# Kernel tuning notes

Hardware: AMD Instinct MI355X
Metric: run time of the kernel (lower is better)

Reference implementation:

```python
import jax, jax.numpy as jnp
import numpy as np

CHUNK = 64
NORM_EPS = 1e-5
DENOM_EPS = 1.0
B, S, HID, H = 4, 4096, 1024, 8
D = HID // H  # 128


def rmsnorm(x, w, eps=NORM_EPS):
    var = jnp.mean(x * x, axis=-1, keepdims=True)
    return x * jax.lax.rsqrt(var + eps) * w


def chunked_linear_attn(q, k, v):
    # q,k,v: [B,S,H,D]; causal linear attention o_s = q_s @ sum_{t<=s} k_t^T v_t
    b, s, h, d = q.shape
    n = s // CHUNK
    def to_chunks(x):
        return x.reshape(b, n, CHUNK, h, d).transpose(1, 0, 3, 2, 4)  # [N,B,H,C,D]
    qc, kc, vc = to_chunks(q), to_chunks(k), to_chunks(v)
    mask = jnp.tril(jnp.ones((CHUNK, CHUNK), dtype=q.dtype))
    def step(state, inp):
        qq, kk, vv = inp  # [B,H,C,D]
        inter = jnp.einsum('bhcd,bhde->bhce', qq, state)
        scores = jnp.einsum('bhcd,bhed->bhce', qq, kk) * mask  # causal intra-chunk
        intra = jnp.einsum('bhce,bhed->bhcd', scores, vv)
        state = state + jnp.einsum('bhcd,bhce->bhde', kk, vv)
        return state, inter + intra
    init = jnp.zeros((b, h, d, d), dtype=q.dtype)
    _, o = jax.lax.scan(step, init, (qc, kc, vc))  # [N,B,H,C,D]
    return o.transpose(1, 0, 3, 2, 4).reshape(b, s, h, d)


def setup_inputs() -> dict:
    key = jax.random.key(0)
    k0, k1, k2, k3, k4 = jax.random.split(key, 5)
    hidden_states = jax.random.normal(k0, (B, S, HID), dtype=jnp.float32)
    Wq = jax.random.normal(k1, (HID, HID), dtype=jnp.float32) * 0.02
    Wk = jax.random.normal(k2, (HID, HID), dtype=jnp.float32) * 0.02
    Wv = jax.random.normal(k3, (HID, HID), dtype=jnp.float32) * 0.02
    Wo = jax.random.normal(k4, (HID, HID), dtype=jnp.float32) * 0.02
    norm_w = jnp.ones((D,), dtype=jnp.float32)
    return {"hidden_states": hidden_states, "Wq": Wq, "Wk": Wk, "Wv": Wv, "Wo": Wo, "norm_w": norm_w}


def reference(hidden_states, Wq, Wk, Wv, Wo, norm_w):
    b, s, _ = hidden_states.shape
    q = jnp.einsum('bsd,ed->bse', hidden_states, Wq).reshape(b, s, H, D)
    k = jnp.einsum('bsd,ed->bse', hidden_states, Wk).reshape(b, s, H, D)
    v = jnp.einsum('bsd,ed->bse', hidden_states, Wv).reshape(b, s, H, D)
    # feature_map='identity', norm_q/norm_k=False
    o = chunked_linear_attn(q, k, v)  # [B,S,H,D]
    z = jnp.cumsum(k, axis=1)
    denom = jnp.maximum(jnp.abs(jnp.sum(q * z, axis=-1)), DENOM_EPS)[..., None]
    o = o / denom
    o = rmsnorm(o, norm_w)
    o = o.reshape(b, s, H * D)
    return jnp.einsum('bse,de->bsd', o, Wo)
```

## Files before the change

### kernel.cpp

```cpp
#include <hip/hip_runtime.h>
#include <stdint.h>

typedef __bf16 bf16x8 __attribute__((ext_vector_type(8)));
typedef float  f32x4  __attribute__((ext_vector_type(4)));

static __device__ __forceinline__ void gload16(const void* g, void* l) {
  __builtin_amdgcn_global_load_lds((__attribute__((address_space(1))) void*)g,
                                   (__attribute__((address_space(3))) void*)l,
                                   16, 0, 0);
}

static __device__ __forceinline__ f32x4 mfma16(bf16x8 a, bf16x8 b, f32x4 c) {
  return __builtin_amdgcn_mfma_f32_16x16x32_bf16(a, b, c, 0, 0, 0);
}

__global__ __launch_bounds__(256) void cast8_k(const float* __restrict__ in,
                                               __bf16* __restrict__ out) {
  const size_t i = ((size_t)blockIdx.x * 256 + threadIdx.x) * 8;
  const float4 v0 = *(const float4*)(in + i);
  const float4 v1 = *(const float4*)(in + i + 4);
  bf16x8 o;
  o[0] = (__bf16)v0.x; o[1] = (__bf16)v0.y; o[2] = (__bf16)v0.z; o[3] = (__bf16)v0.w;
  o[4] = (__bf16)v1.x; o[5] = (__bf16)v1.y; o[6] = (__bf16)v1.z; o[7] = (__bf16)v1.w;
  *(bf16x8*)(out + i) = o;
}

__global__ __launch_bounds__(256) void castw_k(const float* __restrict__ w0, const float* __restrict__ w1,
                                               const float* __restrict__ w2, const float* __restrict__ w3,
                                               __bf16* __restrict__ o0, __bf16* __restrict__ o1,
                                               __bf16* __restrict__ o2, __bf16* __restrict__ o3) {
  const float* in; __bf16* out;
  switch (blockIdx.y) {
    case 0: in = w0; out = o0; break;
    case 1: in = w1; out = o1; break;
    case 2: in = w2; out = o2; break;
    default: in = w3; out = o3; break;
  }
  const size_t i = ((size_t)blockIdx.x * 256 + threadIdx.x) * 8;
  const float4 v0 = *(const float4*)(in + i);
  const float4 v1 = *(const float4*)(in + i + 4);
  bf16x8 o;
  o[0] = (__bf16)v0.x; o[1] = (__bf16)v0.y; o[2] = (__bf16)v0.z; o[3] = (__bf16)v0.w;
  o[4] = (__bf16)v1.x; o[5] = (__bf16)v1.y; o[6] = (__bf16)v1.z; o[7] = (__bf16)v1.w;
  *(bf16x8*)(out + i) = o;
}

__global__ __launch_bounds__(256)
void gemm_qkv_k(const __bf16* __restrict__ A,
                const __bf16* __restrict__ Bq, const __bf16* __restrict__ Bk, const __bf16* __restrict__ Bv,
                __bf16* __restrict__ Qo, __bf16* __restrict__ Ko,
                __bf16* __restrict__ Kt, __bf16* __restrict__ Vt) {
  alignas(16) __shared__ __bf16 sh[128 * 136];
  __bf16* As = sh;
  __bf16* Bs = sh + 128 * 32;
  __bf16* Ts = sh;

  const int tid = threadIdx.x;
  const int flat = blockIdx.x + (blockIdx.y << 3) + (blockIdx.z << 10);
  const int sf = (flat & 7) * 384 + (flat >> 3);
  const int z = sf >> 10;
  const int rem = sf & 1023;
  const int m0 = (rem >> 3) * 128;
  const int n0 = (rem & 7) * 128;

  const __bf16* W = (z == 0) ? Bq : (z == 1) ? Bk : Bv;
  const int l = tid & 63, w = tid >> 6;
  const int wr = (w >> 1) * 64, wc = (w & 1) * 64;
  const int lr = l & 15, lk = (l >> 4) * 8;
  const int srow = tid >> 2, scol = (tid & 3) * 8;

  f32x4 acc[4][4] = {};
  for (int k0 = 0; k0 < 1024; k0 += 32) {
    gload16(A + (size_t)(m0 + srow) * 1024 + k0 + scol, &As[srow * 32 + scol]);
    gload16(A + (size_t)(m0 + 64 + srow) * 1024 + k0 + scol, &As[(64 + srow) * 32 + scol]);
    gload16(W + (size_t)(n0 + srow) * 1024 + k0 + scol, &Bs[srow * 32 + scol]);
    gload16(W + (size_t)(n0 + 64 + srow) * 1024 + k0 + scol, &Bs[(64 + srow) * 32 + scol]);
    __syncthreads();
    bf16x8 af[4], bfr[4];
#pragma unroll
    for (int mt = 0; mt < 4; ++mt) af[mt] = *(const bf16x8*)&As[(wr + mt * 16 + lr) * 32 + lk];
#pragma unroll
    for (int nt = 0; nt < 4; ++nt) bfr[nt] = *(const bf16x8*)&Bs[(wc + nt * 16 + lr) * 32 + lk];
#pragma unroll
    for (int mt = 0; mt < 4; ++mt)
#pragma unroll
      for (int nt = 0; nt < 4; ++nt)
        acc[mt][nt] = mfma16(af[mt], bfr[nt], acc[mt][nt]);
    __syncthreads();
  }

  if (z <= 1) {
    __bf16* R = (z == 0) ? Qo : Ko;
#pragma unroll
    for (int mt = 0; mt < 4; ++mt)
#pragma unroll
      for (int r = 0; r < 4; ++r) {
        const int m = m0 + wr + mt * 16 + (l >> 4) * 4 + r;
#pragma unroll
        for (int nt = 0; nt < 4; ++nt)
          R[(size_t)m * 1024 + n0 + wc + nt * 16 + lr] = (__bf16)acc[mt][nt][r];
      }
  }
  if (z >= 1) {
#pragma unroll
    for (int mt = 0; mt < 4; ++mt)
#pragma unroll
      for (int r = 0; r < 4; ++r) {
        const int m = wr + mt * 16 + (l >> 4) * 4 + r;
#pragma unroll
        for (int nt = 0; nt < 4; ++nt) {
          const int n = wc + nt * 16 + lr;
          Ts[n * 136 + m] = (__bf16)acc[mt][nt][r];
        }
      }
    __syncthreads();
    const int bb = m0 >> 12, s0 = m0 & 4095, hh = n0 >> 7;
    __bf16* T = (z == 1) ? Kt : Vt;
    const size_t tbase = ((size_t)((bb * 8 + hh) * 128)) * 4096 + s0;
#pragma unroll
    for (int it = 0; it < 8; ++it) {
      const int dd = it * 16 + (tid >> 4), s8 = (tid & 15) * 8;
      *(bf16x8*)(T + tbase + (size_t)dd * 4096 + s8) = *(const bf16x8*)&Ts[dd * 136 + s8];
    }
  }
}

__global__ __launch_bounds__(256)
void gemm_out_k(const __bf16* __restrict__ A, const __bf16* __restrict__ W,
                float* __restrict__ Co) {
  alignas(16) __shared__ __bf16 As[128 * 32];
  alignas(16) __shared__ __bf16 Bs[128 * 32];
  const int tid = threadIdx.x;
  const int flat = blockIdx.x + (blockIdx.y << 3);
  const int sf = (flat & 7) * 128 + (flat >> 3);
  const int m0 = (sf >> 3) * 128;
  const int n0 = (sf & 7) * 128;
  const int l = tid & 63, w = tid >> 6;
  const int wr = (w >> 1) * 64, wc = (w & 1) * 64;
  const int lr = l & 15, lk = (l >> 4) * 8;
  const int srow = tid >> 2, scol = (tid & 3) * 8;

  f32x4 acc[4][4] = {};
  for (int k0 = 0; k0 < 1024; k0 += 32) {
    gload16(A + (size_t)(m0 + srow) * 1024 + k0 + scol, &As[srow * 32 + scol]);
    gload16(A + (size_t)(m0 + 64 + srow) * 1024 + k0 + scol, &As[(64 + srow) * 32 + scol]);
    gload16(W + (size_t)(n0 + srow) * 1024 + k0 + scol, &Bs[srow * 32 + scol]);
    gload16(W + (size_t)(n0 + 64 + srow) * 1024 + k0 + scol, &Bs[(64 + srow) * 32 + scol]);
    __syncthreads();
    bf16x8 af[4], bfr[4];
#pragma unroll
    for (int mt = 0; mt < 4; ++mt) af[mt] = *(const bf16x8*)&As[(wr + mt * 16 + lr) * 32 + lk];
#pragma unroll
    for (int nt = 0; nt < 4; ++nt) bfr[nt] = *(const bf16x8*)&Bs[(wc + nt * 16 + lr) * 32 + lk];
#pragma unroll
    for (int mt = 0; mt < 4; ++mt)
#pragma unroll
      for (int nt = 0; nt < 4; ++nt)
        acc[mt][nt] = mfma16(af[mt], bfr[nt], acc[mt][nt]);
    __syncthreads();
  }
#pragma unroll
  for (int mt = 0; mt < 4; ++mt)
#pragma unroll
    for (int r = 0; r < 4; ++r) {
      const int m = m0 + wr + mt * 16 + (l >> 4) * 4 + r;
#pragma unroll
      for (int nt = 0; nt < 4; ++nt) {
        const int n = n0 + wc + nt * 16 + lr;
        Co[(size_t)m * 1024 + n] = acc[mt][nt][r];
      }
    }
}

__global__ __launch_bounds__(128)
void z1_k(const __bf16* __restrict__ K, float* __restrict__ zc) {
  const int c = blockIdx.x, bh = blockIdx.y;
  const int bb = bh >> 3, hh = bh & 7;
  const int d = threadIdx.x;
  float a = 0.0f;
  for (int t = 0; t < 64; ++t)
    a += (float)K[((size_t)(bb * 4096 + c * 64 + t)) * 1024 + hh * 128 + d];
  zc[(size_t)(bh * 64 + c) * 128 + d] = a;
}

__global__ __launch_bounds__(128)
void z2_k(float* __restrict__ zc) {
  const int bh = blockIdx.x;
  const int d = threadIdx.x;
  float run = 0.0f;
  for (int cc = 0; cc < 64; ++cc) {
    float* p = zc + (size_t)(bh * 64 + cc) * 128 + d;
    const float old = *p;
    *p = run;
    run += old;
  }
}

__global__ __launch_bounds__(256)
void passA_k(const __bf16* __restrict__ Kt, const __bf16* __restrict__ Vt,
             __bf16* __restrict__ Sc) {
  const int c = blockIdx.x, bh = blockIdx.y;
  const int tid = threadIdx.x, l = tid & 63, w = tid >> 6;
  const int wr = (w >> 1) * 64, wc = (w & 1) * 64;
  const int lr = l & 15, lk = (l >> 4) * 8;
  f32x4 acc[4][4] = {};
#pragma unroll
  for (int kk = 0; kk < 2; ++kk) {
    const int t = c * 64 + kk * 32 + lk;
    bf16x8 av[4], bk[4];
#pragma unroll
    for (int mt = 0; mt < 4; ++mt)
      av[mt] = *(const bf16x8*)(Vt + ((size_t)(bh * 128 + wr + mt * 16 + lr)) * 4096 + t);
#pragma unroll
    for (int nt = 0; nt < 4; ++nt)
      bk[nt] = *(const bf16x8*)(Kt + ((size_t)(bh * 128 + wc + nt * 16 + lr)) * 4096 + t);
#pragma unroll
    for (int mt = 0; mt < 4; ++mt)
#pragma unroll
      for (int nt = 0; nt < 4; ++nt)
        acc[mt][nt] = mfma16(av[mt], bk[nt], acc[mt][nt]);
  }
  const size_t sbase = ((size_t)(bh * 64 + c)) << 14;
#pragma unroll
  for (int mt = 0; mt < 4; ++mt)
#pragma unroll
    for (int r = 0; r < 4; ++r) {
      const int e = wr + mt * 16 + (l >> 4) * 4 + r;
#pragma unroll
      for (int nt = 0; nt < 4; ++nt) {
        const int d = wc + nt * 16 + lr;
        Sc[sbase + (size_t)e * 128 + d] = (__bf16)acc[mt][nt][r];
      }
    }
}

__global__ __launch_bounds__(256)
void passB_k(__bf16* __restrict__ Sc) {
  const int bh = blockIdx.y;
  const int idx = blockIdx.x * 256 + threadIdx.x;
  float run = 0.0f;
  for (int cc = 0; cc < 64; ++cc) {
    __bf16* p = Sc + (((size_t)(bh * 64 + cc)) << 14) + idx;
    const float old = (float)*p;
    *p = (__bf16)run;
    run += old;
  }
}

__global__ __launch_bounds__(256)
void passC_k(const __bf16* __restrict__ Q, const __bf16* __restrict__ K,
             const __bf16* __restrict__ Vt, const __bf16* __restrict__ Sp,
             const float* __restrict__ zp, const float* __restrict__ nw,
             __bf16* __restrict__ O) {
  alignas(16) __shared__ __bf16 ScL[64 * 72];
  alignas(16) __shared__ float OL[64 * 132];
  alignas(16) __shared__ float zPL[128];
  alignas(16) __shared__ float nwL[128];
  alignas(16) __shared__ float dnL[64];
  const int c = blockIdx.x, bh = blockIdx.y;
  const int bb = bh >> 3, hh = bh & 7;
  const int tid = threadIdx.x, l = tid & 63, wv = tid >> 6;
  const int lr = l & 15, lk = (l >> 4) * 8;
  if (tid < 128) zPL[tid] = zp[(size_t)(bh * 64 + c) * 128 + tid];
  else nwL[tid - 128] = nw[tid - 128];

  const size_t qbase = ((size_t)(bb * 4096 + c * 64)) * 1024 + hh * 128;
  const size_t sbase = ((size_t)(bh * 64 + c)) << 14;

  f32x4 accO[4][2] = {};
  f32x4 accS[4] = {};
#pragma unroll
  for (int kk = 0; kk < 4; ++kk) {
    const int dof = kk * 32 + lk;
    bf16x8 aQ[4], bS[2], bK;
#pragma unroll
    for (int mt = 0; mt < 4; ++mt)
      aQ[mt] = *(const bf16x8*)(Q + qbase + (size_t)(mt * 16 + lr) * 1024 + dof);
#pragma unroll
    for (int nt = 0; nt < 2; ++nt)
      bS[nt] = *(const bf16x8*)(Sp + sbase + (size_t)(wv * 32 + nt * 16 + lr) * 128 + dof);
    bK = *(const bf16x8*)(K + qbase + (size_t)(wv * 16 + lr) * 1024 + dof);
#pragma unroll
    for (int mt = 0; mt < 4; ++mt) {
      accS[mt] = mfma16(aQ[mt], bK, accS[mt]);
#pragma unroll
      for (int nt = 0; nt < 2; ++nt)
        accO[mt][nt] = mfma16(aQ[mt], bS[nt], accO[mt][nt]);
    }
  }
#pragma unroll
  for (int mt = 0; mt < 4; ++mt)
#pragma unroll
    for (int r = 0; r < 4; ++r) {
      const int srow = mt * 16 + (l >> 4) * 4 + r;
      const int tcol = wv * 16 + lr;
      ScL[srow * 72 + tcol] = (__bf16)((tcol <= srow) ? accS[mt][r] : 0.0f);
    }
  __syncthreads();
#pragma unroll
  for (int kk2 = 0; kk2 < 2; ++kk2) {
    const int tof = kk2 * 32 + lk;
    bf16x8 aS[4], bV[2];
#pragma unroll
    for (int mt = 0; mt < 4; ++mt) aS[mt] = *(const bf16x8*)&ScL[(mt * 16 + lr) * 72 + tof];
#pragma unroll
    for (int nt = 0; nt < 2; ++nt)
      bV[nt] = *(const bf16x8*)(Vt + ((size_t)(bh * 128 + wv * 32 + nt * 16 + lr)) * 4096 + c * 64 + tof);
#pragma unroll
    for (int mt = 0; mt < 4; ++mt)
#pragma unroll
      for (int nt = 0; nt < 2; ++nt)
        accO[mt][nt] = mfma16(aS[mt], bV[nt], accO[mt][nt]);
  }
  if (tid < 64) {
    float rs = 0.0f;
    for (int t = 0; t < 64; ++t) rs += (float)ScL[tid * 72 + t];
    float qz = 0.0f;
    const __bf16* qrow = Q + qbase + (size_t)tid * 1024;
#pragma unroll
    for (int j = 0; j < 16; ++j) {
      const bf16x8 q8 = *(const bf16x8*)(qrow + j * 8);
#pragma unroll
      for (int i = 0; i < 8; ++i) qz += (float)q8[i] * zPL[j * 8 + i];
    }
    dnL[tid] = fmaxf(fabsf(qz + rs), 1.0f);
  }
  __syncthreads();
#pragma unroll
  for (int mt = 0; mt < 4; ++mt)
#pragma unroll
    for (int r = 0; r < 4; ++r) {
      const int row = mt * 16 + (l >> 4) * 4 + r;
#pragma unroll
      for (int nt = 0; nt < 2; ++nt) {
        const int col = wv * 32 + nt * 16 + lr;
        OL[row * 132 + col] = accO[mt][nt][r] / dnL[row];
      }
    }
  __syncthreads();
  const int s = tid >> 2, e0 = (tid & 3) * 32;
  float ss = 0.0f;
  for (int i = 0; i < 32; ++i) { const float v = OL[s * 132 + e0 + i]; ss += v * v; }
  ss += __shfl_xor(ss, 1);
  ss += __shfl_xor(ss, 2);
  const float scale = rsqrtf(ss * (1.0f / 128.0f) + 1e-5f);
  __bf16* orow = O + qbase + (size_t)s * 1024 + e0;
#pragma unroll
  for (int i8 = 0; i8 < 4; ++i8) {
    bf16x8 ov;
#pragma unroll
    for (int j = 0; j < 8; ++j) {
      const int e = e0 + i8 * 8 + j;
      ov[j] = (__bf16)(OL[s * 132 + e] * scale * nwL[e]);
    }
    *(bf16x8*)(orow + i8 * 8) = ov;
  }
}

extern "C" void kernel_launch(void* const* d_in, const int* in_sizes, int n_in,
                              void* d_out, int out_size, void* d_ws, size_t ws_size,
                              hipStream_t stream) {
  (void)in_sizes; (void)n_in; (void)out_size; (void)ws_size;
  const float* hid = (const float*)d_in[0];
  const float* Wq  = (const float*)d_in[1];
  const float* Wk  = (const float*)d_in[2];
  const float* Wv  = (const float*)d_in[3];
  const float* Wo  = (const float*)d_in[4];
  const float* nw  = (const float*)d_in[5];

  char* ws = (char*)d_ws;
  size_t off = 0;
  auto nxt = [&](size_t bytes) -> char* {
    char* p = ws + off;
    off += (bytes + 255) & ~(size_t)255;
    return p;
  };
  __bf16* hA  = (__bf16*)nxt(33554432);
  __bf16* wqB = (__bf16*)nxt(2097152);
  __bf16* wkB = (__bf16*)nxt(2097152);
  __bf16* wvB = (__bf16*)nxt(2097152);
  __bf16* woB = (__bf16*)nxt(2097152);
  __bf16* Qb  = (__bf16*)nxt(33554432);
  __bf16* Kb  = (__bf16*)nxt(33554432);
  __bf16* Ktb = (__bf16*)nxt(33554432);
  __bf16* Vtb = (__bf16*)nxt(33554432);
  __bf16* Scb = (__bf16*)nxt(67108864);
  float*  zcb = (float*)nxt(1048576);
  __bf16* Ob  = hA;

  cast8_k<<<8192, 256, 0, stream>>>(hid, hA);
  castw_k<<<dim3(512, 4), 256, 0, stream>>>(Wq, Wk, Wv, Wo, wqB, wkB, wvB, woB);
  gemm_qkv_k<<<dim3(8, 128, 3), 256, 0, stream>>>(hA, wqB, wkB, wvB, Qb, Kb, Ktb, Vtb);
  z1_k<<<dim3(64, 32), 128, 0, stream>>>(Kb, zcb);
  passA_k<<<dim3(64, 32), 256, 0, stream>>>(Ktb, Vtb, Scb);
  passB_k<<<dim3(64, 32), 256, 0, stream>>>(Scb);
  z2_k<<<32, 128, 0, stream>>>(zcb);
  passC_k<<<dim3(64, 32), 256, 0, stream>>>(Qb, Kb, Vtb, Scb, zcb, nw, Ob);
  gemm_out_k<<<dim3(8, 128), 256, 0, stream>>>(Ob, woB, (float*)d_out);
}
```

Baseline: 418.7 us.

## Replace QKV and output GEMMs with 256x256 double-buffered pipelined MFMA kernels

The QKV and output projection GEMMs move from 128x128 tiles with a single LDS buffer and K-step 32 to 256x256 tiles with 512 threads and K-step 64. The new kernels use double-buffered, XOR-swizzled LDS loaded via global_load_lds, with the MFMA work split into four phases interleaved with prefetch, explicit waitcnt/barriers and setprio. The epilogue now stages results through LDS for coalesced 16-byte stores. The goal is more data reuse per tile and overlap of global loads with MFMA. In exchange it needs 128KB of dynamic LDS and heavy register use, and hand-tuned synchronization that is risky to get wrong.

```diff
diff --git a/kernel.cpp b/kernel.cpp
--- a/kernel.cpp
+++ b/kernel.cpp
@@ -13,6 +13,8 @@
 static __device__ __forceinline__ f32x4 mfma16(bf16x8 a, bf16x8 b, f32x4 c) {
   return __builtin_amdgcn_mfma_f32_16x16x32_bf16(a, b, c, 0, 0, 0);
 }
+
+#define MEMFENCE asm volatile("" ::: "memory")
 
 __global__ __launch_bounds__(256) void cast8_k(const float* __restrict__ in,
                                                __bf16* __restrict__ out) {
@@ -45,131 +47,240 @@
   *(bf16x8*)(out + i) = o;
 }
 
-__global__ __launch_bounds__(256)
-void gemm_qkv_k(const __bf16* __restrict__ A,
-                const __bf16* __restrict__ Bq, const __bf16* __restrict__ Bk, const __bf16* __restrict__ Bv,
-                __bf16* __restrict__ Qo, __bf16* __restrict__ Ko,
-                __bf16* __restrict__ Kt, __bf16* __restrict__ Vt) {
-  alignas(16) __shared__ __bf16 sh[128 * 136];
-  __bf16* As = sh;
-  __bf16* Bs = sh + 128 * 32;
-  __bf16* Ts = sh;
-
+static __device__ __forceinline__ void kloop256(
+    const __bf16* __restrict__ A, const __bf16* __restrict__ W,
+    int m0, int n0, __bf16* sh, int tid, f32x4 acc[8][4]) {
+  const int l = tid & 63;
+  const int wv = tid >> 6;
+  const int wm = wv >> 2, wn = wv & 3;
+  const int lo = l & 15, kq = l >> 4;
+
+  auto SA = [&](int kt, int h) {
+#pragma unroll
+    for (int j = 0; j < 2; ++j) {
+      const int p = j * 512 + tid;
+      const int r = p >> 3, sl = p & 7;
+      const int grow = m0 + h * 64 + (r & 63) + (r >> 6) * 128;
+      gload16(A + (size_t)grow * 1024 + (kt << 6) + ((sl ^ (r & 7)) << 3),
+              sh + (kt & 1) * 32768 + h * 8192 + p * 8);
+    }
+  };
+  auto SB = [&](int kt, int h) {
+#pragma unroll
+    for (int j = 0; j < 2; ++j) {
+      const int p = j * 512 + tid;
+      const int r = p >> 3, sl = p & 7;
+      const int grow = n0 + h * 32 + (r & 31) + (r >> 5) * 64;
+      gload16(W + (size_t)grow * 1024 + (kt << 6) + ((sl ^ (r & 7)) << 3),
+              sh + (kt & 1) * 32768 + 16384 + h * 8192 + p * 8);
+    }
+  };
+  auto LDA = [&](int cur, int mh, int mi, int ks) -> bf16x8 {
+    const int r = wm * 64 + mi * 16 + lo;
+    return *(const bf16x8*)&sh[cur * 32768 + mh * 8192 + r * 64 + (((ks * 4 + kq) ^ (r & 7)) << 3)];
+  };
+  auto LDB = [&](int cur, int nh, int ni, int ks) -> bf16x8 {
+    const int r = wn * 32 + ni * 16 + lo;
+    return *(const bf16x8*)&sh[cur * 32768 + 16384 + nh * 8192 + r * 64 + (((ks * 4 + kq) ^ (r & 7)) << 3)];
+  };
+
+  SA(0, 0); SB(0, 0); SB(0, 1); SA(0, 1);
+  SA(1, 0); SB(1, 1); SA(1, 1);
+  MEMFENCE;
+  asm volatile("s_waitcnt vmcnt(6)" ::: "memory");
+  __builtin_amdgcn_s_barrier();
+
+  bf16x8 a[4][2], b[2][2], b2[2][2];
+#pragma unroll 2
+  for (int t = 0; t < 16; ++t) {
+    const int cur = t & 1;
+#pragma unroll
+    for (int mi = 0; mi < 4; ++mi)
+#pragma unroll
+      for (int ks = 0; ks < 2; ++ks) a[mi][ks] = LDA(cur, 0, mi, ks);
+#pragma unroll
+    for (int ni = 0; ni < 2; ++ni)
+#pragma unroll
+      for (int ks = 0; ks < 2; ++ks) b[ni][ks] = LDB(cur, 0, ni, ks);
+    if (t + 1 < 16) SB(t + 1, 0);
+    MEMFENCE;
+    __builtin_amdgcn_s_barrier();
+    asm volatile("s_waitcnt lgkmcnt(0)" ::: "memory");
+    __builtin_amdgcn_sched_barrier(0);
+    __builtin_amdgcn_s_setprio(1);
+#pragma unroll
+    for (int mi = 0; mi < 4; ++mi)
+#pragma unroll
+      for (int ni = 0; ni < 2; ++ni)
+#pragma unroll
+        for (int ks = 0; ks < 2; ++ks)
+          acc[mi][ni] = mfma16(a[mi][ks], b[ni][ks], acc[mi][ni]);
+    __builtin_amdgcn_s_setprio(0);
+    MEMFENCE;
+    __builtin_amdgcn_s_barrier();
+#pragma unroll
+    for (int ni = 0; ni < 2; ++ni)
+#pragma unroll
+      for (int ks = 0; ks < 2; ++ks) b2[ni][ks] = LDB(cur, 1, ni, ks);
+    if (t + 2 < 16) SA(t + 2, 0);
+    MEMFENCE;
+    __builtin_amdgcn_s_barrier();
+    asm volatile("s_waitcnt lgkmcnt(0)" ::: "memory");
+    __builtin_amdgcn_sched_barrier(0);
+    __builtin_amdgcn_s_setprio(1);
+#pragma unroll
+    for (int mi = 0; mi < 4; ++mi)
+#pragma unroll
+      for (int ni = 0; ni < 2; ++ni)
+#pragma unroll
+        for (int ks = 0; ks < 2; ++ks)
+          acc[mi][2 + ni] = mfma16(a[mi][ks], b2[ni][ks], acc[mi][2 + ni]);
+    __builtin_amdgcn_s_setprio(0);
+    MEMFENCE;
+    __builtin_amdgcn_s_barrier();
+#pragma unroll
+    for (int mi = 0; mi < 4; ++mi)
+#pragma unroll
+      for (int ks = 0; ks < 2; ++ks) a[mi][ks] = LDA(cur, 1, mi, ks);
+    if (t + 2 < 16) SB(t + 2, 1);
+    MEMFENCE;
+    __builtin_amdgcn_s_barrier();
+    asm volatile("s_waitcnt lgkmcnt(0)" ::: "memory");
+    __builtin_amdgcn_sched_barrier(0);
+    __builtin_amdgcn_s_setprio(1);
+#pragma unroll
+    for (int mi = 0; mi < 4; ++mi)
+#pragma unroll
+      for (int ni = 0; ni < 2; ++ni)
+#pragma unroll
+        for (int ks = 0; ks < 2; ++ks)
+          acc[4 + mi][2 + ni] = mfma16(a[mi][ks], b2[ni][ks], acc[4 + mi][2 + ni]);
+    __builtin_amdgcn_s_setprio(0);
+    MEMFENCE;
+    __builtin_amdgcn_s_barrier();
+#pragma unroll
+    for (int ni = 0; ni < 2; ++ni)
+#pragma unroll
+      for (int ks = 0; ks < 2; ++ks) b[ni][ks] = LDB(cur, 0, ni, ks);
+    if (t + 2 < 16) SA(t + 2, 1);
+    MEMFENCE;
+    __builtin_amdgcn_s_barrier();
+    asm volatile("s_waitcnt lgkmcnt(0)" ::: "memory");
+    __builtin_amdgcn_sched_barrier(0);
+    __builtin_amdgcn_s_setprio(1);
+#pragma unroll
+    for (int mi = 0; mi < 4; ++mi)
+#pragma unroll
+      for (int ni = 0; ni < 2; ++ni)
+#pragma unroll
+        for (int ks = 0; ks < 2; ++ks)
+          acc[4 + mi][ni] = mfma16(a[mi][ks], b[ni][ks], acc[4 + mi][ni]);
+    __builtin_amdgcn_s_setprio(0);
+    if (t < 14) asm volatile("s_waitcnt vmcnt(6)" ::: "memory");
+    else        asm volatile("s_waitcnt vmcnt(0)" ::: "memory");
+    MEMFENCE;
+    __builtin_amdgcn_s_barrier();
+  }
+}
+
+__global__ __launch_bounds__(512, 2)
+void gemm_qkv8_k(const __bf16* __restrict__ A,
+                 const __bf16* __restrict__ Bq, const __bf16* __restrict__ Bk, const __bf16* __restrict__ Bv,
+                 __bf16* __restrict__ Qo, __bf16* __restrict__ Ko,
+                 __bf16* __restrict__ Kt, __bf16* __restrict__ Vt) {
+  extern __shared__ __bf16 sh[];
   const int tid = threadIdx.x;
-  const int flat = blockIdx.x + (blockIdx.y << 3) + (blockIdx.z << 10);
-  const int sf = (flat & 7) * 384 + (flat >> 3);
-  const int z = sf >> 10;
-  const int rem = sf & 1023;
-  const int m0 = (rem >> 3) * 128;
-  const int n0 = (rem & 7) * 128;
-
+  const int flat = blockIdx.x;
+  const int sf = (flat & 7) * 96 + (flat >> 3);
+  const int z = sf >> 8;
+  const int rem = sf & 255;
+  const int m0 = (rem >> 2) * 256;
+  const int n0 = (rem & 3) * 256;
   const __bf16* W = (z == 0) ? Bq : (z == 1) ? Bk : Bv;
-  const int l = tid & 63, w = tid >> 6;
-  const int wr = (w >> 1) * 64, wc = (w & 1) * 64;
-  const int lr = l & 15, lk = (l >> 4) * 8;
-  const int srow = tid >> 2, scol = (tid & 3) * 8;
-
-  f32x4 acc[4][4] = {};
-  for (int k0 = 0; k0 < 1024; k0 += 32) {
-    gload16(A + (size_t)(m0 + srow) * 1024 + k0 + scol, &As[srow * 32 + scol]);
-    gload16(A + (size_t)(m0 + 64 + srow) * 1024 + k0 + scol, &As[(64 + srow) * 32 + scol]);
-    gload16(W + (size_t)(n0 + srow) * 1024 + k0 + scol, &Bs[srow * 32 + scol]);
-    gload16(W + (size_t)(n0 + 64 + srow) * 1024 + k0 + scol, &Bs[(64 + srow) * 32 + scol]);
-    __syncthreads();
-    bf16x8 af[4], bfr[4];
-#pragma unroll
-    for (int mt = 0; mt < 4; ++mt) af[mt] = *(const bf16x8*)&As[(wr + mt * 16 + lr) * 32 + lk];
-#pragma unroll
-    for (int nt = 0; nt < 4; ++nt) bfr[nt] = *(const bf16x8*)&Bs[(wc + nt * 16 + lr) * 32 + lk];
-#pragma unroll
-    for (int mt = 0; mt < 4; ++mt)
-#pragma unroll
-      for (int nt = 0; nt < 4; ++nt)
-        acc[mt][nt] = mfma16(af[mt], bfr[nt], acc[mt][nt]);
-    __syncthreads();
-  }
+
+  f32x4 acc[8][4] = {};
+  kloop256(A, W, m0, n0, sh, tid, acc);
+
+  const int l = tid & 63, wv = tid >> 6, wm = wv >> 2, wn = wv & 3;
+  const int lo = l & 15, kq = l >> 4;
 
   if (z <= 1) {
-    __bf16* R = (z == 0) ? Qo : Ko;
-#pragma unroll
-    for (int mt = 0; mt < 4; ++mt)
-#pragma unroll
-      for (int r = 0; r < 4; ++r) {
-        const int m = m0 + wr + mt * 16 + (l >> 4) * 4 + r;
-#pragma unroll
-        for (int nt = 0; nt < 4; ++nt)
-          R[(size_t)m * 1024 + n0 + wc + nt * 16 + lr] = (__bf16)acc[mt][nt][r];
+    __bf16* R = z ? Ko : Qo;
+#pragma unroll
+    for (int nh = 0; nh < 2; ++nh) {
+      if ((wn >> 1) == nh) {
+#pragma unroll
+        for (int mi = 0; mi < 8; ++mi)
+#pragma unroll
+          for (int ni = 0; ni < 4; ++ni)
+#pragma unroll
+            for (int rr = 0; rr < 4; ++rr)
+              sh[wm * 17408 + (mi * 16 + kq * 4 + rr) * 136 + (wn & 1) * 64 + ni * 16 + lo]
+                  = (__bf16)acc[mi][ni][rr];
       }
+      __syncthreads();
+#pragma unroll
+      for (int it = 0; it < 8; ++it) {
+        const int idx = it * 512 + tid;
+        const int rg = idx >> 11, mrow = (idx >> 4) & 127, sl = idx & 15;
+        *(bf16x8*)(R + (size_t)(m0 + rg * 128 + mrow) * 1024 + n0 + nh * 128 + sl * 8)
+            = *(const bf16x8*)&sh[rg * 17408 + mrow * 136 + sl * 8];
+      }
+      __syncthreads();
+    }
   }
   if (z >= 1) {
-#pragma unroll
-    for (int mt = 0; mt < 4; ++mt)
-#pragma unroll
-      for (int r = 0; r < 4; ++r) {
-        const int m = wr + mt * 16 + (l >> 4) * 4 + r;
-#pragma unroll
-        for (int nt = 0; nt < 4; ++nt) {
-          const int n = wc + nt * 16 + lr;
-          Ts[n * 136 + m] = (__bf16)acc[mt][nt][r];
-        }
+    __bf16* T = (z == 1) ? Kt : Vt;
+    const int bb = m0 >> 12, s0v = m0 & 4095, h0 = n0 >> 7;
+#pragma unroll
+    for (int nh = 0; nh < 2; ++nh) {
+      if ((wn >> 1) == nh) {
+#pragma unroll
+        for (int mi = 0; mi < 8; ++mi)
+#pragma unroll
+          for (int ni = 0; ni < 4; ++ni)
+#pragma unroll
+            for (int rr = 0; rr < 4; ++rr)
+              sh[wm * 17408 + ((wn & 1) * 64 + ni * 16 + lo) * 136 + mi * 16 + kq * 4 + rr]
+                  = (__bf16)acc[mi][ni][rr];
       }
-    __syncthreads();
-    const int bb = m0 >> 12, s0 = m0 & 4095, hh = n0 >> 7;
-    __bf16* T = (z == 1) ? Kt : Vt;
-    const size_t tbase = ((size_t)((bb * 8 + hh) * 128)) * 4096 + s0;
-#pragma unroll
-    for (int it = 0; it < 8; ++it) {
-      const int dd = it * 16 + (tid >> 4), s8 = (tid & 15) * 8;
-      *(bf16x8*)(T + tbase + (size_t)dd * 4096 + s8) = *(const bf16x8*)&Ts[dd * 136 + s8];
-    }
-  }
-}
-
-__global__ __launch_bounds__(256)
-void gemm_out_k(const __bf16* __restrict__ A, const __bf16* __restrict__ W,
-                float* __restrict__ Co) {
-  alignas(16) __shared__ __bf16 As[128 * 32];
-  alignas(16) __shared__ __bf16 Bs[128 * 32];
+      __syncthreads();
+      const int hh = h0 + nh;
+#pragma unroll
+      for (int it = 0; it < 8; ++it) {
+        const int idx = it * 512 + tid;
+        const int rg = idx >> 11, dr = (idx >> 4) & 127, sl = idx & 15;
+        *(bf16x8*)(T + ((size_t)((bb * 8 + hh) * 128 + dr)) * 4096 + s0v + rg * 128 + sl * 8)
+            = *(const bf16x8*)&sh[rg * 17408 + dr * 136 + sl * 8];
+      }
+      __syncthreads();
+    }
+  }
+}
+
+__global__ __launch_bounds__(512, 2)
+void gemm_out8_k(const __bf16* __restrict__ A, const __bf16* __restrict__ W,
+                 float* __restrict__ Co) {
+  extern __shared__ __bf16 sh[];
   const int tid = threadIdx.x;
-  const int flat = blockIdx.x + (blockIdx.y << 3);
-  const int sf = (flat & 7) * 128 + (flat >> 3);
-  const int m0 = (sf >> 3) * 128;
-  const int n0 = (sf & 7) * 128;
-  const int l = tid & 63, w = tid >> 6;
-  const int wr = (w >> 1) * 64, wc = (w & 1) * 64;
-  const int lr = l & 15, lk = (l >> 4) * 8;
-  const int srow = tid >> 2, scol = (tid & 3) * 8;
-
-  f32x4 acc[4][4] = {};
-  for (int k0 = 0; k0 < 1024; k0 += 32) {
-    gload16(A + (size_t)(m0 + srow) * 1024 + k0 + scol, &As[srow * 32 + scol]);
-    gload16(A + (size_t)(m0 + 64 + srow) * 1024 + k0 + scol, &As[(64 + srow) * 32 + scol]);
-    gload16(W + (size_t)(n0 + srow) * 1024 + k0 + scol, &Bs[srow * 32 + scol]);
-    gload16(W + (size_t)(n0 + 64 + srow) * 1024 + k0 + scol, &Bs[(64 + srow) * 32 + scol]);
-    __syncthreads();
-    bf16x8 af[4], bfr[4];
-#pragma unroll
-    for (int mt = 0; mt < 4; ++mt) af[mt] = *(const bf16x8*)&As[(wr + mt * 16 + lr) * 32 + lk];
-#pragma unroll
-    for (int nt = 0; nt < 4; ++nt) bfr[nt] = *(const bf16x8*)&Bs[(wc + nt * 16 + lr) * 32 + lk];
-#pragma unroll
-    for (int mt = 0; mt < 4; ++mt)
-#pragma unroll
-      for (int nt = 0; nt < 4; ++nt)
-        acc[mt][nt] = mfma16(af[mt], bfr[nt], acc[mt][nt]);
-    __syncthreads();
-  }
-#pragma unroll
-  for (int mt = 0; mt < 4; ++mt)
-#pragma unroll
-    for (int r = 0; r < 4; ++r) {
-      const int m = m0 + wr + mt * 16 + (l >> 4) * 4 + r;
-#pragma unroll
-      for (int nt = 0; nt < 4; ++nt) {
-        const int n = n0 + wc + nt * 16 + lr;
-        Co[(size_t)m * 1024 + n] = acc[mt][nt][r];
-      }
-    }
+  const int flat = blockIdx.x;
+  const int sf = (flat & 7) * 32 + (flat >> 3);
+  const int m0 = (sf >> 2) * 256;
+  const int n0 = (sf & 3) * 256;
+
+  f32x4 acc[8][4] = {};
+  kloop256(A, W, m0, n0, sh, tid, acc);
+
+  const int l = tid & 63, wv = tid >> 6, wm = wv >> 2, wn = wv & 3;
+  const int lo = l & 15, kq = l >> 4;
+#pragma unroll
+  for (int mi = 0; mi < 8; ++mi)
+#pragma unroll
+    for (int ni = 0; ni < 4; ++ni)
+#pragma unroll
+      for (int rr = 0; rr < 4; ++rr)
+        Co[(size_t)(m0 + wm * 128 + mi * 16 + kq * 4 + rr) * 1024 + n0 + wn * 64 + ni * 16 + lo]
+            = acc[mi][ni][rr];
 }
 
 __global__ __launch_bounds__(128)
@@ -390,11 +501,11 @@
 
   cast8_k<<<8192, 256, 0, stream>>>(hid, hA);
   castw_k<<<dim3(512, 4), 256, 0, stream>>>(Wq, Wk, Wv, Wo, wqB, wkB, wvB, woB);
-  gemm_qkv_k<<<dim3(8, 128, 3), 256, 0, stream>>>(hA, wqB, wkB, wvB, Qb, Kb, Ktb, Vtb);
+  gemm_qkv8_k<<<768, 512, 131072, stream>>>(hA, wqB, wkB, wvB, Qb, Kb, Ktb, Vtb);
   z1_k<<<dim3(64, 32), 128, 0, stream>>>(Kb, zcb);
   passA_k<<<dim3(64, 32), 256, 0, stream>>>(Ktb, Vtb, Scb);
   passB_k<<<dim3(64, 32), 256, 0, stream>>>(Scb);
   z2_k<<<32, 128, 0, stream>>>(zcb);
   passC_k<<<dim3(64, 32), 256, 0, stream>>>(Qb, Kb, Vtb, Scb, zcb, nw, Ob);
-  gemm_out_k<<<dim3(8, 128), 256, 0, stream>>>(Ob, woB, (float*)d_out);
-}
+  gemm_out8_k<<<256, 512, 131072, stream>>>(Ob, woB, (float*)d_out);
+}
```

Result: faster. 385.7 us (-7.9%).
